# Kernel optimization log

Hardware: AMD Instinct MI355X
Metric: run time of the kernel (lower is better)

The kernel has to match this reference:

```python
import jax, jax.numpy as jnp
import numpy as np

DIM = 1024
HEADS = 16
HEAD_DIM = DIM // HEADS // 2  # 32
DEPTH = 12
LAMBDA_INIT = 0.8 - 0.6 * float(np.exp(-0.3 * DEPTH))
EPS = 1e-5
B, N = 2, 2048


def setup_inputs() -> dict:
    key = jax.random.key(0)
    ks = jax.random.split(key, 9)
    s = 0.02
    return {
        "x": jax.random.normal(ks[0], (B, N, DIM), jnp.float32),
        "W_qkv": jax.random.normal(ks[1], (DIM, 3 * DIM), jnp.float32) * s,
        "W_proj": jax.random.normal(ks[2], (DIM, DIM), jnp.float32) * s,
        "b_proj": jnp.zeros((DIM,), jnp.float32),
        "lambda_q1": jax.random.normal(ks[3], (HEAD_DIM,), jnp.float32) * 0.1,
        "lambda_k1": jax.random.normal(ks[4], (HEAD_DIM,), jnp.float32) * 0.1,
        "lambda_q2": jax.random.normal(ks[5], (HEAD_DIM,), jnp.float32) * 0.1,
        "lambda_k2": jax.random.normal(ks[6], (HEAD_DIM,), jnp.float32) * 0.1,
        "subln_w": jnp.ones((2 * HEAD_DIM,), jnp.float32),
    }


def reference(x, W_qkv, W_proj, b_proj, lambda_q1, lambda_k1, lambda_q2, lambda_k2, subln_w):
    Bm, Nm, C = x.shape
    H, hd = HEADS, HEAD_DIM
    scale = hd ** -0.5

    qkv = (x @ W_qkv).reshape(Bm, Nm, 3, H, 2 * hd)
    q, k, v = qkv[:, :, 0], qkv[:, :, 1], qkv[:, :, 2]
    # split each head's 2*hd dims into two sub-heads -> [B, 2H, N, hd]
    q = q.reshape(Bm, Nm, 2 * H, hd).transpose(0, 2, 1, 3)
    k = k.reshape(Bm, Nm, 2 * H, hd).transpose(0, 2, 1, 3)
    v = v.transpose(0, 2, 1, 3)  # [B, H, N, 2*hd]

    q1, q2 = q[:, :H], q[:, H:]
    k1, k2 = k[:, :H], k[:, H:]

    def sdpa(qh, kh):
        scores = jnp.einsum('bhqd,bhkd->bhqk', qh, kh) * scale
        a = jax.nn.softmax(scores, axis=-1)
        return jnp.einsum('bhqk,bhkd->bhqd', a, v)  # [B,H,N,2*hd]

    attn1 = sdpa(q1, k1)
    attn2 = sdpa(q2, k2)

    lam1 = jnp.exp(jnp.sum(lambda_q1 * lambda_k1))
    lam2 = jnp.exp(jnp.sum(lambda_q2 * lambda_k2))
    lam = lam1 - lam2 + LAMBDA_INIT

    o = attn1 - lam * attn2  # [B,H,N,2*hd]
    # RMSNorm over last dim (2*hd) with elementwise affine
    o = o * jax.lax.rsqrt(jnp.mean(o * o, axis=-1, keepdims=True) + EPS)
    o = o * subln_w
    o = o * (1.0 - LAMBDA_INIT)

    o = o.transpose(0, 2, 1, 3).reshape(Bm, Nm, C)
    return o @ W_proj + b_proj
```

## Files before the change

### kernel.cpp

```cpp
#include <hip/hip_runtime.h>

typedef unsigned short ushort_t;
typedef unsigned int uint_t;
typedef __attribute__((ext_vector_type(4))) float f32x4;
typedef __attribute__((ext_vector_type(8))) __bf16 bf16x8;

#define LAMBDA_INIT 0.7836057665316245f
#define ONE_MINUS_LI 0.21639423346837552f
#define QSCALE_LOG2E 0.25505654442552663f

__device__ inline ushort_t f2bf(float f) {
  union { float f; unsigned u; } v; v.f = f;
  unsigned r = (v.u + 0x7FFFu + ((v.u >> 16) & 1u)) >> 16;
  return (ushort_t)r;
}

__device__ inline float fexp2(float x) {
  float r;
  asm("v_exp_f32 %0, %1" : "=v"(r) : "v"(x));
  return r;
}

__device__ inline uint_t cvtpk(float lo, float hi) {
  uint_t r;
  asm("v_cvt_pk_bf16_f32 %0, %1, %2" : "=v"(r) : "v"(lo), "v"(hi));
  return r;
}

__device__ inline f32x4 zero4() { f32x4 z = {0.f, 0.f, 0.f, 0.f}; return z; }

__device__ inline f32x4 mfma16(bf16x8 a, bf16x8 b, f32x4 c) {
  return __builtin_amdgcn_mfma_f32_16x16x32_bf16(a, b, c, 0, 0, 0);
}

__device__ inline void gload_lds16(const void* g, void* l) {
  __builtin_amdgcn_global_load_lds(
      (const __attribute__((address_space(1))) unsigned int*)g,
      (__attribute__((address_space(3))) unsigned int*)l, 16, 0, 0);
}

__global__ __launch_bounds__(256) void cvt_f32_bf16(const float* __restrict__ in,
                                                    ushort_t* __restrict__ out, int n) {
  int i = (blockIdx.x * 256 + threadIdx.x) * 8;
  if (i >= n) return;
  float4 a = *(const float4*)(in + i);
  float4 b = *(const float4*)(in + i + 4);
  uint4 pack;
  pack.x = cvtpk(a.x, a.y);
  pack.y = cvtpk(a.z, a.w);
  pack.z = cvtpk(b.x, b.y);
  pack.w = cvtpk(b.z, b.w);
  *(uint4*)(out + i) = pack;
}

__global__ __launch_bounds__(256) void transpose_to_bf16(const float* __restrict__ W,
                                                         ushort_t* __restrict__ WT,
                                                         int K, int N) {
  __shared__ float tile[32][33];
  int n0 = blockIdx.x * 32, k0 = blockIdx.y * 32;
  int tx = threadIdx.x & 31, ty = threadIdx.x >> 5;
#pragma unroll
  for (int j = 0; j < 4; ++j) {
    int k = k0 + ty + j * 8;
    tile[ty + j * 8][tx] = W[(size_t)k * N + n0 + tx];
  }
  __syncthreads();
#pragma unroll
  for (int j = 0; j < 4; ++j) {
    int n = n0 + ty + j * 8;
    WT[(size_t)n * K + k0 + tx] = f2bf(tile[tx][ty + j * 8]);
  }
}

template <int MODE>
__global__ __launch_bounds__(256) void gemm_bt(const ushort_t* __restrict__ A,
                                               const ushort_t* __restrict__ Bt,
                                               void* __restrict__ C,
                                               ushort_t* __restrict__ vt_out,
                                               const float* __restrict__ bias,
                                               int M, int N, int K) {
  __shared__ ushort_t As[128 * 32];
  __shared__ ushort_t Bs[128 * 32];
  const int tid = threadIdx.x;
  const int wave = tid >> 6, lane = tid & 63;
  const int wr = wave >> 1, wc = wave & 1;
  const int lg = lane >> 4, ll = lane & 15;

  const int lin = blockIdx.x + gridDim.x * blockIdx.y;
  const int cpx = (gridDim.x * gridDim.y) >> 3;
  const int swz = (lin & 7) * cpx + (lin >> 3);
  const int row0 = (swz % gridDim.x) * 128, col0 = (swz / gridDim.x) * 128;

  f32x4 acc[4][4];
#pragma unroll
  for (int m = 0; m < 4; ++m)
#pragma unroll
    for (int n = 0; n < 4; ++n) acc[m][n] = zero4();

  for (int k0 = 0; k0 < K; k0 += 32) {
    __syncthreads();
#pragma unroll
    for (int i = 0; i < 2; ++i) {
      int c = tid + i * 256;
      int r = c >> 2, ko = (c & 3) << 3;
      gload_lds16(A + (size_t)(row0 + r) * K + k0 + ko,
                  (char*)As + (size_t)(wave * 64 + i * 256) * 16);
      gload_lds16(Bt + (size_t)(col0 + r) * K + k0 + ko,
                  (char*)Bs + (size_t)(wave * 64 + i * 256) * 16);
    }
    __syncthreads();
    bf16x8 af[4], bf[4];
#pragma unroll
    for (int m = 0; m < 4; ++m)
      af[m] = *(const bf16x8*)(As + (wr * 64 + m * 16 + ll) * 32 + (lg << 3));
#pragma unroll
    for (int n = 0; n < 4; ++n)
      bf[n] = *(const bf16x8*)(Bs + (wc * 64 + n * 16 + ll) * 32 + (lg << 3));
#pragma unroll
    for (int m = 0; m < 4; ++m)
#pragma unroll
      for (int n = 0; n < 4; ++n) acc[m][n] = mfma16(af[m], bf[n], acc[m][n]);
  }

#pragma unroll
  for (int m = 0; m < 4; ++m) {
#pragma unroll
    for (int n = 0; n < 4; ++n) {
      int gc = col0 + wc * 64 + n * 16 + ll;
      int gr0 = row0 + wr * 64 + m * 16 + (lg << 2);
      if (MODE == 0) {
#pragma unroll
        for (int j = 0; j < 4; ++j)
          ((float*)C)[(size_t)(gr0 + j) * N + gc] = acc[m][n][j] + bias[gc];
      } else {
        if (gc < 2048) {
          float sc = (gc < 1024) ? QSCALE_LOG2E : 1.0f;
#pragma unroll
          for (int j = 0; j < 4; ++j)
            ((ushort_t*)C)[(size_t)(gr0 + j) * 2048 + gc] = f2bf(acc[m][n][j] * sc);
        } else {
          int hv = (gc - 2048) >> 6, dv = (gc - 2048) & 63;
          int bb = gr0 >> 11, nn = gr0 & 2047;
          uint2 w;
          w.x = cvtpk(acc[m][n][0], acc[m][n][1]);
          w.y = cvtpk(acc[m][n][2], acc[m][n][3]);
          *(uint2*)(vt_out + ((size_t)((bb * 16 + hv) * 64 + dv)) * 2048 + nn) = w;
        }
      }
    }
  }
}

__global__ __launch_bounds__(512) void diff_attn(const ushort_t* __restrict__ qk,
                                                 const ushort_t* __restrict__ vt,
                                                 ushort_t* __restrict__ o,
                                                 const float* __restrict__ lq1,
                                                 const float* __restrict__ lk1,
                                                 const float* __restrict__ lq2,
                                                 const float* __restrict__ lk2,
                                                 const float* __restrict__ subln) {
  const int lin = blockIdx.x + (blockIdx.y << 4) + (blockIdx.z << 8);
  const int swz = ((lin & 7) << 6) + (lin >> 3);
  const int qt = swz & 15, h = (swz >> 4) & 15, b = swz >> 8;
  const int tid = threadIdx.x, wave = tid >> 6, lane = tid & 63;
  const int lg = lane >> 4, ll = lane & 15;

  const size_t qbase = (size_t)b * 2048 * 2048;
  const int cq1 = (h << 5), cq2 = 512 + (h << 5);
  const int ck1 = 1024 + (h << 5), ck2 = 1536 + (h << 5);
  const size_t vbase = (size_t)((b * 16 + h) * 64) * 2048;

  float sl1 = 0.f, sl2 = 0.f;
  for (int j = 0; j < 32; ++j) { sl1 += lq1[j] * lk1[j]; sl2 += lq2[j] * lk2[j]; }
  const float lam = __expf(sl1) - __expf(sl2) + LAMBDA_INIT;

  __shared__ ushort_t Ks[2][64 * 64];
  __shared__ ushort_t Vs[2][64 * 64];
  __shared__ ushort_t Pl[8][2][16 * 72];

  const int qrow = qt * 128 + wave * 16 + ll;
  const bf16x8 q1f = *(const bf16x8*)(qk + qbase + (size_t)qrow * 2048 + cq1 + (lg << 3));
  const bf16x8 q2f = *(const bf16x8*)(qk + qbase + (size_t)qrow * 2048 + cq2 + (lg << 3));

  f32x4 o1[4], o2[4];
#pragma unroll
  for (int nb = 0; nb < 4; ++nb) { o1[nb] = zero4(); o2[nb] = zero4(); }
  float l1p = 0.f, l2p = 0.f;
  ushort_t* Pw0 = &Pl[wave][0][0];
  ushort_t* Pw1 = &Pl[wave][1][0];

  const int r0 = tid >> 3, c0 = (tid & 7) ^ (r0 & 7);
  const int kc0 = ((c0 & 4) ? ck2 : ck1) + ((c0 & 3) << 3);
  const int ub0 = tid << 4;

#define STAGE(buf, kv0)                                                                   \
  do {                                                                                    \
    gload_lds16(qk + qbase + (size_t)((kv0) + r0) * 2048 + kc0, (char*)Ks[buf] + ub0);    \
    gload_lds16(vt + vbase + (size_t)r0 * 2048 + (kv0) + (c0 << 3), (char*)Vs[buf] + ub0);\
  } while (0)

  auto compute_tile = [&](const ushort_t* Kc, const ushort_t* Vc) {
    bf16x8 vf[2][4];
#pragma unroll
    for (int ks = 0; ks < 2; ++ks)
#pragma unroll
      for (int nb = 0; nb < 4; ++nb)
        vf[ks][nb] = *(const bf16x8*)(Vc + nb * 1024 + ll * 64 + (((ks * 4 + lg) ^ (ll & 7)) << 3));
#pragma unroll
    for (int pass = 0; pass < 2; ++pass) {
      const int cK = (lg ^ (ll & 7)) ^ (pass << 2);
      ushort_t* Pw = pass ? Pw1 : Pw0;
      bf16x8 kf[4];
#pragma unroll
      for (int nb = 0; nb < 4; ++nb)
        kf[nb] = *(const bf16x8*)(Kc + nb * 1024 + ll * 64 + (cK << 3));
      const bf16x8 qf = pass ? q2f : q1f;
      f32x4* oacc = pass ? o2 : o1;
      f32x4 s[4];
      __builtin_amdgcn_s_setprio(1);
#pragma unroll
      for (int nb = 0; nb < 4; ++nb)
        s[nb] = mfma16(kf[nb], qf, zero4());
      __builtin_amdgcn_s_setprio(0);
      float part = 0.f;
#pragma unroll
      for (int nb = 0; nb < 4; ++nb) {
        float e0 = fexp2(s[nb][0]), e1 = fexp2(s[nb][1]);
        float e2 = fexp2(s[nb][2]), e3 = fexp2(s[nb][3]);
        part += (e0 + e1) + (e2 + e3);
        uint2 w;
        w.x = cvtpk(e0, e1);
        w.y = cvtpk(e2, e3);
        *(uint2*)(Pw + ll * 72 + nb * 16 + (lg << 2)) = w;
      }
      if (pass) l2p += part; else l1p += part;
      __builtin_amdgcn_s_setprio(1);
#pragma unroll
      for (int ks = 0; ks < 2; ++ks) {
        bf16x8 pf = *(const bf16x8*)(Pw + ll * 72 + ks * 32 + (lg << 3));
#pragma unroll
        for (int nb = 0; nb < 4; ++nb) oacc[nb] = mfma16(pf, vf[ks][nb], oacc[nb]);
      }
      __builtin_amdgcn_s_setprio(0);
    }
  };

  STAGE(0, 0);
  __syncthreads();
  for (int tt = 0; tt < 16; ++tt) {
    STAGE(1, (tt * 2 + 1) * 64);
    compute_tile(Ks[0], Vs[0]);
    __syncthreads();
    if (tt < 15) STAGE(0, (tt * 2 + 2) * 64);
    compute_tile(Ks[1], Vs[1]);
    __syncthreads();
  }
#undef STAGE

  float l1 = l1p; l1 += __shfl_xor(l1, 16); l1 += __shfl_xor(l1, 32);
  float l2 = l2p; l2 += __shfl_xor(l2, 16); l2 += __shfl_xor(l2, 32);
  float i1[4], i2[4];
#pragma unroll
  for (int j = 0; j < 4; ++j) {
    int src = (lane & 48) | ((lg << 2) + j);
    i1[j] = 1.f / __shfl(l1, src);
    i2[j] = 1.f / __shfl(l2, src);
  }

  float ss[4] = {0.f, 0.f, 0.f, 0.f};
  f32x4 ov[4];
#pragma unroll
  for (int nb = 0; nb < 4; ++nb) {
#pragma unroll
    for (int j = 0; j < 4; ++j) {
      float x = o1[nb][j] * i1[j] - lam * (o2[nb][j] * i2[j]);
      ov[nb][j] = x;
      ss[j] += x * x;
    }
  }
#pragma unroll
  for (int mask = 1; mask < 16; mask <<= 1)
#pragma unroll
    for (int j = 0; j < 4; ++j) ss[j] += __shfl_xor(ss[j], mask);
  float nf[4];
#pragma unroll
  for (int j = 0; j < 4; ++j) nf[j] = rsqrtf(ss[j] * (1.f / 64.f) + 1e-5f);
  const size_t orow0 = (size_t)(b * 2048 + qt * 128 + wave * 16);
#pragma unroll
  for (int nb = 0; nb < 4; ++nb) {
    int d = nb * 16 + ll;
    float sw = subln[d] * ONE_MINUS_LI;
#pragma unroll
    for (int j = 0; j < 4; ++j) {
      int r = (lg << 2) + j;
      o[(orow0 + r) * 1024 + (h << 6) + d] = f2bf(ov[nb][j] * nf[j] * sw);
    }
  }
}

extern "C" void kernel_launch(void* const* d_in, const int* in_sizes, int n_in,
                              void* d_out, int out_size, void* d_ws, size_t ws_size,
                              hipStream_t stream) {
  const float* x      = (const float*)d_in[0];
  const float* W_qkv  = (const float*)d_in[1];
  const float* W_proj = (const float*)d_in[2];
  const float* b_proj = (const float*)d_in[3];
  const float* lq1    = (const float*)d_in[4];
  const float* lk1    = (const float*)d_in[5];
  const float* lq2    = (const float*)d_in[6];
  const float* lk2    = (const float*)d_in[7];
  const float* subln  = (const float*)d_in[8];

  char* ws = (char*)d_ws;
  ushort_t* xb     = (ushort_t*)(ws);
  ushort_t* qkb    = (ushort_t*)(ws + 8388608);
  ushort_t* vtb    = (ushort_t*)(ws + 25165824);
  ushort_t* wqkvT  = (ushort_t*)(ws + 33554432);
  ushort_t* wprojT = (ushort_t*)(ws + 39845888);
  ushort_t* ob     = (ushort_t*)(ws + 41943040);

  cvt_f32_bf16<<<2048, 256, 0, stream>>>(x, xb, 4096 * 1024);
  transpose_to_bf16<<<dim3(96, 32), 256, 0, stream>>>(W_qkv, wqkvT, 1024, 3072);
  transpose_to_bf16<<<dim3(32, 32), 256, 0, stream>>>(W_proj, wprojT, 1024, 1024);
  gemm_bt<1><<<dim3(32, 24), 256, 0, stream>>>(xb, wqkvT, (void*)qkb, vtb, nullptr, 4096, 3072, 1024);
  diff_attn<<<dim3(16, 16, 2), 512, 0, stream>>>(qkb, vtb, ob, lq1, lk1, lq2, lk2, subln);
  gemm_bt<0><<<dim3(32, 8), 256, 0, stream>>>(ob, wprojT, d_out, nullptr, b_proj, 4096, 1024, 1024);
}
```

Measured before the change: 170.5 us.

## Triple-buffer K/V tiles with one barrier per tile and vmcnt waits

Replaces the double-buffered K/V staging, which used two __syncthreads per pair of tiles, with a three-slot ring buffer. Prefetch runs two tiles ahead, and each tile starts with one s_waitcnt vmcnt plus a raw s_barrier. The per-wave P scratch shrinks from two buffers to one shared by both passes. The aim is to cut barrier count and hide global-to-LDS latency better, at the cost of more LDS for K/V. Reusing a single P buffer across passes relies on in-wave ordering, which carries some hazard risk.

```diff
diff --git a/kernel.cpp b/kernel.cpp
--- a/kernel.cpp
+++ b/kernel.cpp
@@ -174,9 +174,9 @@
   for (int j = 0; j < 32; ++j) { sl1 += lq1[j] * lk1[j]; sl2 += lq2[j] * lk2[j]; }
   const float lam = __expf(sl1) - __expf(sl2) + LAMBDA_INIT;
 
-  __shared__ ushort_t Ks[2][64 * 64];
-  __shared__ ushort_t Vs[2][64 * 64];
-  __shared__ ushort_t Pl[8][2][16 * 72];
+  __shared__ ushort_t Ks[3][64 * 64];
+  __shared__ ushort_t Vs[3][64 * 64];
+  __shared__ ushort_t Pl[8][16 * 72];
 
   const int qrow = qt * 128 + wave * 16 + ll;
   const bf16x8 q1f = *(const bf16x8*)(qk + qbase + (size_t)qrow * 2048 + cq1 + (lg << 3));
@@ -186,8 +186,7 @@
 #pragma unroll
   for (int nb = 0; nb < 4; ++nb) { o1[nb] = zero4(); o2[nb] = zero4(); }
   float l1p = 0.f, l2p = 0.f;
-  ushort_t* Pw0 = &Pl[wave][0][0];
-  ushort_t* Pw1 = &Pl[wave][1][0];
+  ushort_t* Pw = &Pl[wave][0];
 
   const int r0 = tid >> 3, c0 = (tid & 7) ^ (r0 & 7);
   const int kc0 = ((c0 & 4) ? ck2 : ck1) + ((c0 & 3) << 3);
@@ -209,7 +208,6 @@
 #pragma unroll
     for (int pass = 0; pass < 2; ++pass) {
       const int cK = (lg ^ (ll & 7)) ^ (pass << 2);
-      ushort_t* Pw = pass ? Pw1 : Pw0;
       bf16x8 kf[4];
 #pragma unroll
       for (int nb = 0; nb < 4; ++nb)
@@ -246,15 +244,26 @@
   };
 
   STAGE(0, 0);
-  __syncthreads();
-  for (int tt = 0; tt < 16; ++tt) {
-    STAGE(1, (tt * 2 + 1) * 64);
-    compute_tile(Ks[0], Vs[0]);
-    __syncthreads();
-    if (tt < 15) STAGE(0, (tt * 2 + 2) * 64);
-    compute_tile(Ks[1], Vs[1]);
-    __syncthreads();
-  }
+  STAGE(1, 64);
+
+#define TILE(bufc, bufn, t)                                                               \
+  do {                                                                                    \
+    if ((t) < 31) asm volatile("s_waitcnt vmcnt(2)" ::: "memory");                        \
+    else          asm volatile("s_waitcnt vmcnt(0)" ::: "memory");                        \
+    __builtin_amdgcn_s_barrier();                                                         \
+    __builtin_amdgcn_sched_barrier(0);                                                    \
+    compute_tile(Ks[bufc], Vs[bufc]);                                                     \
+    if ((t) + 2 < 32) STAGE(bufn, ((t) + 2) * 64);                                        \
+  } while (0)
+
+  for (int base = 0; base < 30; base += 3) {
+    TILE(0, 2, base);
+    TILE(1, 0, base + 1);
+    TILE(2, 1, base + 2);
+  }
+  TILE(0, 2, 30);
+  TILE(1, 0, 31);
+#undef TILE
 #undef STAGE
 
   float l1 = l1p; l1 += __shfl_xor(l1, 16); l1 += __shfl_xor(l1, 32);
```

New measurement: 159.9 us. -6.2%, faster.
